# Kernel optimization log

Hardware: AMD Instinct MI355X
Metric: run time of the kernel (lower is better)

The kernel has to match this reference:

```python
import jax, jax.numpy as jnp
import numpy as np

N, D = 16384, 512
LOGIT_SCALE = 14.285714  # 1/0.07, standard CLIP temperature


def setup_inputs() -> dict:
    key = jax.random.key(0)
    k1, k2 = jax.random.split(key)
    image_features = jax.random.normal(k1, (N, D), dtype=jnp.float32)
    text_features = jax.random.normal(k2, (N, D), dtype=jnp.float32)
    logit_scale = jnp.asarray(LOGIT_SCALE, dtype=jnp.float32)
    return {
        "image_features": image_features,
        "text_features": text_features,
        "logit_scale": logit_scale,
    }


def reference(image_features, text_features, logit_scale):
    # logits_per_image = scale * img @ txt.T  -> [N, N]
    # logits_per_text is its transpose, so compute the GEMM once.
    logits = logit_scale * jnp.einsum("nd,md->nm", image_features, text_features)
    diag = jnp.diagonal(logits)  # correct-pair logits (labels = arange)
    # cross_entropy with label i on row i: logsumexp(row) - logit[i,i]
    loss_i = jnp.mean(jax.nn.logsumexp(logits, axis=1) - diag)
    # text loss uses transposed logits -> column-wise logsumexp
    loss_t = jnp.mean(jax.nn.logsumexp(logits, axis=0) - diag)
    return (loss_i + loss_t) * 0.5
```

## Files before the change

kernel.cpp:

```cpp
#include <hip/hip_runtime.h>
#include <hip/hip_bf16.h>

#define N_ 16384
#define D_ 512
#define BM 128
#define BN 128
#define BK 64
#define NBLK (N_ / BM)

typedef __attribute__((ext_vector_type(8))) __bf16 bf16x8;
typedef __attribute__((ext_vector_type(4))) float f32x4;

#define GLDS(gptr, lptr)                                                              \
  __builtin_amdgcn_global_load_lds((const __attribute__((address_space(1))) void*)(gptr), \
                                   (__attribute__((address_space(3))) void*)(lptr), 16, 0, 0)

__device__ inline unsigned short f2bf(float f) {
  __hip_bfloat16 h = __float2bfloat16(f);
  return *reinterpret_cast<unsigned short*>(&h);
}

__global__ void cvt_bf16_kernel(const float* __restrict__ src,
                                unsigned short* __restrict__ dst, long n,
                                const float* __restrict__ scale_p) {
  const float s = scale_p ? scale_p[0] : 1.0f;
  long i = ((long)blockIdx.x * blockDim.x + threadIdx.x) * 8;
  const long stride = (long)gridDim.x * blockDim.x * 8;
  typedef __attribute__((ext_vector_type(8))) unsigned short us8;
  for (; i < n; i += stride) {
    const float4* sp = (const float4*)(src + i);
    float4 f0 = sp[0], f1 = sp[1];
    us8 v;
    v[0] = f2bf(f0.x * s); v[1] = f2bf(f0.y * s); v[2] = f2bf(f0.z * s); v[3] = f2bf(f0.w * s);
    v[4] = f2bf(f1.x * s); v[5] = f2bf(f1.y * s); v[6] = f2bf(f1.z * s); v[7] = f2bf(f1.w * s);
    *(us8*)(dst + i) = v;
  }
}

__global__ __launch_bounds__(256, 4)
void gemm_lse_kernel(const unsigned short* __restrict__ A,
                     const unsigned short* __restrict__ B,
                     float2* __restrict__ rowMS,
                     float2* __restrict__ colMS,
                     float* __restrict__ diag) {
  __shared__ unsigned short As[BM][BK];
  __shared__ unsigned short Bs[BN][BK];
  __shared__ float rowbuf[2][BM][2];
  __shared__ float colbuf[2][BN][2];

  const int t = threadIdx.x;
  const int l = t & 63;
  const int wid = t >> 6;
  const int wr = wid >> 1;
  const int wc = wid & 1;

  int id = blockIdx.x;
  id = (id & 7) * (NBLK * NBLK / 8) + (id >> 3);
  const int br = id / NBLK;
  const int bc = id % NBLK;

  const int srow = t >> 3;
  const int scol = (((t & 7) ^ (srow & 7)) << 3);

  f32x4 acc[4][4];
#pragma unroll
  for (int m = 0; m < 4; ++m)
#pragma unroll
    for (int n = 0; n < 4; ++n) acc[m][n] = (f32x4)0.0f;

  const unsigned short* aBase = A + (size_t)(br * BM + srow) * D_ + scol;
  const unsigned short* bBase = B + (size_t)(bc * BN + srow) * D_ + scol;
  char* asBase = (char*)&As[0][0] + t * 16;
  char* bsBase = (char*)&Bs[0][0] + t * 16;

  const int swz = (l & 7) << 4;

  for (int kt = 0; kt < D_ / BK; ++kt) {
    const int k0 = kt * BK;
#pragma unroll
    for (int c = 0; c < 4; ++c) GLDS(aBase + k0 + c * 32 * D_, asBase + c * 4096);
#pragma unroll
    for (int c = 0; c < 4; ++c) GLDS(bBase + k0 + c * 32 * D_, bsBase + c * 4096);
    __syncthreads();
#pragma unroll
    for (int kk = 0; kk < 2; ++kk) {
      const int cb = (kk * 64 + (l >> 4) * 16);
      bf16x8 af[4], bfv[4];
#pragma unroll
      for (int m = 0; m < 4; ++m)
        af[m] = *(const bf16x8*)((const char*)&As[0][0] +
                                 (wr * 64 + m * 16 + (l & 15)) * 128 + (cb ^ swz));
#pragma unroll
      for (int n = 0; n < 4; ++n)
        bfv[n] = *(const bf16x8*)((const char*)&Bs[0][0] +
                                  (wc * 64 + n * 16 + (l & 15)) * 128 + (cb ^ swz));
#pragma unroll
      for (int m = 0; m < 4; ++m)
#pragma unroll
        for (int n = 0; n < 4; ++n)
          acc[m][n] = __builtin_amdgcn_mfma_f32_16x16x32_bf16(af[m], bfv[n], acc[m][n], 0, 0, 0);
    }
    __syncthreads();
  }

  if (br == bc && wr == wc) {
#pragma unroll
    for (int m = 0; m < 4; ++m)
#pragma unroll
      for (int r = 0; r < 4; ++r)
        if ((l & 15) == ((l >> 4) * 4 + r))
          diag[br * BM + wr * 64 + m * 16 + (l & 15)] = acc[m][m][r];
  }

#pragma unroll
  for (int m = 0; m < 4; ++m) {
#pragma unroll
    for (int r = 0; r < 4; ++r) {
      float mx = fmaxf(fmaxf(acc[m][0][r], acc[m][1][r]), fmaxf(acc[m][2][r], acc[m][3][r]));
#pragma unroll
      for (int off = 1; off < 16; off <<= 1) mx = fmaxf(mx, __shfl_xor(mx, off, 64));
      float s = 0.f;
#pragma unroll
      for (int n = 0; n < 4; ++n) s += __expf(acc[m][n][r] - mx);
#pragma unroll
      for (int off = 1; off < 16; off <<= 1) s += __shfl_xor(s, off, 64);
      if ((l & 15) == 0) {
        int row = wr * 64 + m * 16 + (l >> 4) * 4 + r;
        rowbuf[wc][row][0] = mx;
        rowbuf[wc][row][1] = s;
      }
    }
  }

#pragma unroll
  for (int n = 0; n < 4; ++n) {
    float mx = -1e30f;
#pragma unroll
    for (int m = 0; m < 4; ++m)
#pragma unroll
      for (int r = 0; r < 4; ++r) mx = fmaxf(mx, acc[m][n][r]);
    mx = fmaxf(mx, __shfl_xor(mx, 16, 64));
    mx = fmaxf(mx, __shfl_xor(mx, 32, 64));
    float s = 0.f;
#pragma unroll
    for (int m = 0; m < 4; ++m)
#pragma unroll
      for (int r = 0; r < 4; ++r) s += __expf(acc[m][n][r] - mx);
    s += __shfl_xor(s, 16, 64);
    s += __shfl_xor(s, 32, 64);
    if ((l >> 4) == 0) {
      int col = wc * 64 + n * 16 + l;
      colbuf[wr][col][0] = mx;
      colbuf[wr][col][1] = s;
    }
  }
  __syncthreads();

  if (t < BM) {
    float m0 = rowbuf[0][t][0], s0 = rowbuf[0][t][1];
    float m1 = rowbuf[1][t][0], s1 = rowbuf[1][t][1];
    float mm = fmaxf(m0, m1);
    float ss = s0 * __expf(m0 - mm) + s1 * __expf(m1 - mm);
    rowMS[(size_t)bc * N_ + br * BM + t] = make_float2(mm, ss);
  } else {
    int c = t - BM;
    float m0 = colbuf[0][c][0], s0 = colbuf[0][c][1];
    float m1 = colbuf[1][c][0], s1 = colbuf[1][c][1];
    float mm = fmaxf(m0, m1);
    float ss = s0 * __expf(m0 - mm) + s1 * __expf(m1 - mm);
    colMS[(size_t)br * N_ + bc * BN + c] = make_float2(mm, ss);
  }
}

__global__ void reduce1_kernel(const float2* __restrict__ rowMS,
                               const float2* __restrict__ colMS,
                               const float* __restrict__ diag,
                               float* __restrict__ partials) {
  const int tid = blockIdx.x * blockDim.x + threadIdx.x;
  float m = -1e30f, s = 0.f;
  if (tid < N_) {
    const int r = tid;
    for (int cb = 0; cb < NBLK; ++cb) {
      float2 p = rowMS[(size_t)cb * N_ + r];
      float nm = fmaxf(m, p.x);
      s = s * __expf(m - nm) + p.y * __expf(p.x - nm);
      m = nm;
    }
    m = m + logf(s) - diag[r];
  } else {
    const int c = tid - N_;
    for (int rb = 0; rb < NBLK; ++rb) {
      float2 p = colMS[(size_t)rb * N_ + c];
      float nm = fmaxf(m, p.x);
      s = s * __expf(m - nm) + p.y * __expf(p.x - nm);
      m = nm;
    }
    m = m + logf(s) - diag[c];
  }
  float val = m;
#pragma unroll
  for (int off = 1; off < 64; off <<= 1) val += __shfl_xor(val, off, 64);
  __shared__ float red[4];
  if ((threadIdx.x & 63) == 0) red[threadIdx.x >> 6] = val;
  __syncthreads();
  if (threadIdx.x == 0) partials[blockIdx.x] = red[0] + red[1] + red[2] + red[3];
}

__global__ void reduce2_kernel(const float* __restrict__ partials, float* __restrict__ out) {
  const int t = threadIdx.x;
  float v = partials[t] + partials[t + 64];
#pragma unroll
  for (int off = 1; off < 64; off <<= 1) v += __shfl_xor(v, off, 64);
  if (t == 0) out[0] = v * (1.0f / (2.0f * (float)N_));
}

extern "C" void kernel_launch(void* const* d_in, const int* in_sizes, int n_in,
                              void* d_out, int out_size, void* d_ws, size_t ws_size,
                              hipStream_t stream) {
  const float* img = (const float*)d_in[0];
  const float* txt = (const float*)d_in[1];
  const float* scale = (const float*)d_in[2];
  float* out = (float*)d_out;

  char* ws = (char*)d_ws;
  size_t off = 0;
  unsigned short* imgB = (unsigned short*)(ws + off); off += (size_t)N_ * D_ * 2;
  unsigned short* txtB = (unsigned short*)(ws + off); off += (size_t)N_ * D_ * 2;
  float2* rowMS = (float2*)(ws + off); off += (size_t)NBLK * N_ * sizeof(float2);
  float2* colMS = (float2*)(ws + off); off += (size_t)NBLK * N_ * sizeof(float2);
  float* diag = (float*)(ws + off); off += (size_t)N_ * sizeof(float);
  float* partials = (float*)(ws + off); off += 128 * sizeof(float);
  (void)ws_size; (void)in_sizes; (void)n_in; (void)out_size;

  cvt_bf16_kernel<<<1024, 256, 0, stream>>>(img, imgB, (long)N_ * D_, scale);
  cvt_bf16_kernel<<<1024, 256, 0, stream>>>(txt, txtB, (long)N_ * D_, nullptr);
  gemm_lse_kernel<<<NBLK * NBLK, 256, 0, stream>>>(imgB, txtB, rowMS, colMS, diag);
  reduce1_kernel<<<(2 * N_) / 256, 256, 0, stream>>>(rowMS, colMS, diag, partials);
  reduce2_kernel<<<1, 64, 0, stream>>>(partials, out);
}
```

Measured before the change: 408.7 us.

## Enlarge GEMM tile to 256x256 with 512 threads and double-buffered async LDS loads

Grows the block tile from 128x128 to 256x256 using 8 waves, each computing a 128x64 sub-tile. LDS staging is now double-buffered, with a prefetch two k-steps ahead, explicit vmcnt waits and raw barriers, so global-to-LDS copies overlap the MFMA work. MFMA sections also run at raised wave priority. This aims to cut global traffic per FLOP and hide load latency, at the cost of more registers, lower occupancy, and fewer blocks for load balance. The per-tile row/column partial LSE outputs halve in count, and the tail merge now combines four row partials instead of two.

```diff
diff --git a/kernel.cpp b/kernel.cpp
--- a/kernel.cpp
+++ b/kernel.cpp
@@ -3,10 +3,12 @@
 
 #define N_ 16384
 #define D_ 512
-#define BM 128
-#define BN 128
+#define BM 256
+#define BN 256
 #define BK 64
+#define NT (D_ / BK)
 #define NBLK (N_ / BM)
+#define BUFB 32768
 
 typedef __attribute__((ext_vector_type(8))) __bf16 bf16x8;
 typedef __attribute__((ext_vector_type(4))) float f32x4;
@@ -37,22 +39,20 @@
   }
 }
 
-__global__ __launch_bounds__(256, 4)
+__global__ __launch_bounds__(512, 2)
 void gemm_lse_kernel(const unsigned short* __restrict__ A,
                      const unsigned short* __restrict__ B,
                      float2* __restrict__ rowMS,
                      float2* __restrict__ colMS,
                      float* __restrict__ diag) {
-  __shared__ unsigned short As[BM][BK];
-  __shared__ unsigned short Bs[BN][BK];
-  __shared__ float rowbuf[2][BM][2];
-  __shared__ float colbuf[2][BN][2];
+  __shared__ __align__(16) unsigned short As[2][BM][BK];
+  __shared__ __align__(16) unsigned short Bs[2][BN][BK];
 
   const int t = threadIdx.x;
   const int l = t & 63;
   const int wid = t >> 6;
-  const int wr = wid >> 1;
-  const int wc = wid & 1;
+  const int wr = wid >> 2;
+  const int wc = wid & 3;
 
   int id = blockIdx.x;
   id = (id & 7) * (NBLK * NBLK / 8) + (id >> 3);
@@ -62,58 +62,90 @@
   const int srow = t >> 3;
   const int scol = (((t & 7) ^ (srow & 7)) << 3);
 
-  f32x4 acc[4][4];
-#pragma unroll
-  for (int m = 0; m < 4; ++m)
-#pragma unroll
-    for (int n = 0; n < 4; ++n) acc[m][n] = (f32x4)0.0f;
-
   const unsigned short* aBase = A + (size_t)(br * BM + srow) * D_ + scol;
   const unsigned short* bBase = B + (size_t)(bc * BN + srow) * D_ + scol;
-  char* asBase = (char*)&As[0][0] + t * 16;
-  char* bsBase = (char*)&Bs[0][0] + t * 16;
+
+  f32x4 acc[8][4];
+#pragma unroll
+  for (int m = 0; m < 8; ++m)
+#pragma unroll
+    for (int n = 0; n < 4; ++n) acc[m][n] = (f32x4)0.0f;
 
   const int swz = (l & 7) << 4;
-
-  for (int kt = 0; kt < D_ / BK; ++kt) {
-    const int k0 = kt * BK;
-#pragma unroll
-    for (int c = 0; c < 4; ++c) GLDS(aBase + k0 + c * 32 * D_, asBase + c * 4096);
-#pragma unroll
-    for (int c = 0; c < 4; ++c) GLDS(bBase + k0 + c * 32 * D_, bsBase + c * 4096);
-    __syncthreads();
+  const char* asb = (const char*)As;
+  const char* bsb = (const char*)Bs;
+
+#define STAGE(kt_, b_)                                              \
+  {                                                                 \
+    const unsigned short* ag_ = aBase + (kt_)*BK;                   \
+    const unsigned short* bg_ = bBase + (kt_)*BK;                   \
+    char* al_ = (char*)As + (b_)*BUFB + t * 16;                     \
+    char* bl_ = (char*)Bs + (b_)*BUFB + t * 16;                     \
+    _Pragma("unroll") for (int c_ = 0; c_ < 4; ++c_) {              \
+      GLDS(ag_ + c_ * 64 * D_, al_ + c_ * 8192);                    \
+      GLDS(bg_ + c_ * 64 * D_, bl_ + c_ * 8192);                    \
+    }                                                               \
+  }
+
+  STAGE(0, 0);
+  STAGE(1, 1);
+
+#pragma unroll
+  for (int kt = 0; kt < NT; ++kt) {
+    const int b = kt & 1;
+    if (kt == NT - 1) { asm volatile("s_waitcnt vmcnt(0)" ::: "memory"); }
+    else              { asm volatile("s_waitcnt vmcnt(8)" ::: "memory"); }
+    __builtin_amdgcn_sched_barrier(0);
+    __builtin_amdgcn_s_barrier();
+    __builtin_amdgcn_sched_barrier(0);
+
 #pragma unroll
     for (int kk = 0; kk < 2; ++kk) {
-      const int cb = (kk * 64 + (l >> 4) * 16);
-      bf16x8 af[4], bfv[4];
-#pragma unroll
-      for (int m = 0; m < 4; ++m)
-        af[m] = *(const bf16x8*)((const char*)&As[0][0] +
-                                 (wr * 64 + m * 16 + (l & 15)) * 128 + (cb ^ swz));
+      const int cbk = kk * 64 + (l >> 4) * 16;
+      bf16x8 af[8], bfv[4];
+#pragma unroll
+      for (int m = 0; m < 8; ++m)
+        af[m] = *(const bf16x8*)(asb + b * BUFB +
+                                 (wr * 128 + m * 16 + (l & 15)) * 128 + (cbk ^ swz));
 #pragma unroll
       for (int n = 0; n < 4; ++n)
-        bfv[n] = *(const bf16x8*)((const char*)&Bs[0][0] +
-                                  (wc * 64 + n * 16 + (l & 15)) * 128 + (cb ^ swz));
-#pragma unroll
-      for (int m = 0; m < 4; ++m)
+        bfv[n] = *(const bf16x8*)(bsb + b * BUFB +
+                                  (wc * 64 + n * 16 + (l & 15)) * 128 + (cbk ^ swz));
+      __builtin_amdgcn_s_setprio(1);
+#pragma unroll
+      for (int m = 0; m < 8; ++m)
 #pragma unroll
         for (int n = 0; n < 4; ++n)
           acc[m][n] = __builtin_amdgcn_mfma_f32_16x16x32_bf16(af[m], bfv[n], acc[m][n], 0, 0, 0);
-    }
-    __syncthreads();
-  }
-
-  if (br == bc && wr == wc) {
-#pragma unroll
-    for (int m = 0; m < 4; ++m)
-#pragma unroll
-      for (int r = 0; r < 4; ++r)
-        if ((l & 15) == ((l >> 4) * 4 + r))
-          diag[br * BM + wr * 64 + m * 16 + (l & 15)] = acc[m][m][r];
-  }
-
-#pragma unroll
-  for (int m = 0; m < 4; ++m) {
+      __builtin_amdgcn_s_setprio(0);
+    }
+
+    asm volatile("s_waitcnt lgkmcnt(0)" ::: "memory");
+    __builtin_amdgcn_sched_barrier(0);
+    __builtin_amdgcn_s_barrier();
+    __builtin_amdgcn_sched_barrier(0);
+    if (kt + 2 < NT) STAGE(kt + 2, b);
+  }
+#undef STAGE
+
+  float* rowb = (float*)As;
+  float* colb = rowb + 4 * 256 * 2;
+
+  if (br == bc) {
+#pragma unroll
+    for (int m = 0; m < 8; ++m)
+#pragma unroll
+      for (int n = 0; n < 4; ++n)
+#pragma unroll
+        for (int r = 0; r < 4; ++r) {
+          const int row = wr * 128 + m * 16 + (l >> 4) * 4 + r;
+          const int col = wc * 64 + n * 16 + (l & 15);
+          if (row == col) diag[br * BM + row] = acc[m][n][r];
+        }
+  }
+
+#pragma unroll
+  for (int m = 0; m < 8; ++m) {
 #pragma unroll
     for (int r = 0; r < 4; ++r) {
       float mx = fmaxf(fmaxf(acc[m][0][r], acc[m][1][r]), fmaxf(acc[m][2][r], acc[m][3][r]));
@@ -125,9 +157,9 @@
 #pragma unroll
       for (int off = 1; off < 16; off <<= 1) s += __shfl_xor(s, off, 64);
       if ((l & 15) == 0) {
-        int row = wr * 64 + m * 16 + (l >> 4) * 4 + r;
-        rowbuf[wc][row][0] = mx;
-        rowbuf[wc][row][1] = s;
+        const int row = wr * 128 + m * 16 + (l >> 4) * 4 + r;
+        rowb[(wc * 256 + row) * 2 + 0] = mx;
+        rowb[(wc * 256 + row) * 2 + 1] = s;
       }
     }
   }
@@ -136,38 +168,46 @@
   for (int n = 0; n < 4; ++n) {
     float mx = -1e30f;
 #pragma unroll
-    for (int m = 0; m < 4; ++m)
+    for (int m = 0; m < 8; ++m)
 #pragma unroll
       for (int r = 0; r < 4; ++r) mx = fmaxf(mx, acc[m][n][r]);
     mx = fmaxf(mx, __shfl_xor(mx, 16, 64));
     mx = fmaxf(mx, __shfl_xor(mx, 32, 64));
     float s = 0.f;
 #pragma unroll
-    for (int m = 0; m < 4; ++m)
+    for (int m = 0; m < 8; ++m)
 #pragma unroll
       for (int r = 0; r < 4; ++r) s += __expf(acc[m][n][r] - mx);
     s += __shfl_xor(s, 16, 64);
     s += __shfl_xor(s, 32, 64);
     if ((l >> 4) == 0) {
-      int col = wc * 64 + n * 16 + l;
-      colbuf[wr][col][0] = mx;
-      colbuf[wr][col][1] = s;
+      const int col = wc * 64 + n * 16 + l;
+      colb[(wr * 256 + col) * 2 + 0] = mx;
+      colb[(wr * 256 + col) * 2 + 1] = s;
     }
   }
   __syncthreads();
 
-  if (t < BM) {
-    float m0 = rowbuf[0][t][0], s0 = rowbuf[0][t][1];
-    float m1 = rowbuf[1][t][0], s1 = rowbuf[1][t][1];
-    float mm = fmaxf(m0, m1);
-    float ss = s0 * __expf(m0 - mm) + s1 * __expf(m1 - mm);
+  if (t < 256) {
+    float mm = -1e30f, ss = 0.f;
+#pragma unroll
+    for (int w = 0; w < 4; ++w) {
+      float m0 = rowb[(w * 256 + t) * 2 + 0], s0 = rowb[(w * 256 + t) * 2 + 1];
+      float nm = fmaxf(mm, m0);
+      ss = ss * __expf(mm - nm) + s0 * __expf(m0 - nm);
+      mm = nm;
+    }
     rowMS[(size_t)bc * N_ + br * BM + t] = make_float2(mm, ss);
   } else {
-    int c = t - BM;
-    float m0 = colbuf[0][c][0], s0 = colbuf[0][c][1];
-    float m1 = colbuf[1][c][0], s1 = colbuf[1][c][1];
-    float mm = fmaxf(m0, m1);
-    float ss = s0 * __expf(m0 - mm) + s1 * __expf(m1 - mm);
+    const int c = t - 256;
+    float mm = -1e30f, ss = 0.f;
+#pragma unroll
+    for (int w = 0; w < 2; ++w) {
+      float m0 = colb[(w * 256 + c) * 2 + 0], s0 = colb[(w * 256 + c) * 2 + 1];
+      float nm = fmaxf(mm, m0);
+      ss = ss * __expf(mm - nm) + s0 * __expf(m0 - nm);
+      mm = nm;
+    }
     colMS[(size_t)br * N_ + bc * BN + c] = make_float2(mm, ss);
   }
 }
@@ -234,7 +274,7 @@
 
   cvt_bf16_kernel<<<1024, 256, 0, stream>>>(img, imgB, (long)N_ * D_, scale);
   cvt_bf16_kernel<<<1024, 256, 0, stream>>>(txt, txtB, (long)N_ * D_, nullptr);
-  gemm_lse_kernel<<<NBLK * NBLK, 256, 0, stream>>>(imgB, txtB, rowMS, colMS, diag);
+  gemm_lse_kernel<<<NBLK * NBLK, 512, 0, stream>>>(imgB, txtB, rowMS, colMS, diag);
   reduce1_kernel<<<(2 * N_) / 256, 256, 0, stream>>>(rowMS, colMS, diag, partials);
   reduce2_kernel<<<1, 64, 0, stream>>>(partials, out);
 }
```

Measured after the change: 468.7 us. 1.15x slower.

## Double-buffer GEMM LDS tiles with BK=32 and switch LSE to base-2 exponent

Applied to the files above, without the earlier changes.

Halves the K tile to 32 and double-buffers the A/B shared tiles, so the next tile's global-to-LDS load is issued before the MFMAs on the current one. This cuts one barrier per K step and sets wave priority around the MFMA block. It also drops the XOR swizzle, which may bring LDS bank conflicts back on the fragment reads. Separately, log2(e) is folded into the bf16 conversion scale so every exp/log becomes exp2f/log2f, and the result is converted back with ln2 at the end.

```diff
diff --git a/kernel.cpp b/kernel.cpp
--- a/kernel.cpp
+++ b/kernel.cpp
@@ -5,8 +5,10 @@
 #define D_ 512
 #define BM 128
 #define BN 128
-#define BK 64
+#define BK 32
+#define NT (D_ / BK)
 #define NBLK (N_ / BM)
+#define BUFB 8192
 
 typedef __attribute__((ext_vector_type(8))) __bf16 bf16x8;
 typedef __attribute__((ext_vector_type(4))) float f32x4;
@@ -15,6 +17,8 @@
   __builtin_amdgcn_global_load_lds((const __attribute__((address_space(1))) void*)(gptr), \
                                    (__attribute__((address_space(3))) void*)(lptr), 16, 0, 0)
 
+#define MFMA16(a, b, c) __builtin_amdgcn_mfma_f32_16x16x32_bf16((a), (b), (c), 0, 0, 0)
+
 __device__ inline unsigned short f2bf(float f) {
   __hip_bfloat16 h = __float2bfloat16(f);
   return *reinterpret_cast<unsigned short*>(&h);
@@ -23,7 +27,7 @@
 __global__ void cvt_bf16_kernel(const float* __restrict__ src,
                                 unsigned short* __restrict__ dst, long n,
                                 const float* __restrict__ scale_p) {
-  const float s = scale_p ? scale_p[0] : 1.0f;
+  const float s = scale_p ? scale_p[0] * 1.4426950408889634f : 1.0f;
   long i = ((long)blockIdx.x * blockDim.x + threadIdx.x) * 8;
   const long stride = (long)gridDim.x * blockDim.x * 8;
   typedef __attribute__((ext_vector_type(8))) unsigned short us8;
@@ -43,8 +47,8 @@
                      float2* __restrict__ rowMS,
                      float2* __restrict__ colMS,
                      float* __restrict__ diag) {
-  __shared__ unsigned short As[BM][BK];
-  __shared__ unsigned short Bs[BN][BK];
+  __shared__ __align__(16) unsigned short As[2][BM][BK];
+  __shared__ __align__(16) unsigned short Bs[2][BN][BK];
   __shared__ float rowbuf[2][BM][2];
   __shared__ float colbuf[2][BN][2];
 
@@ -59,49 +63,54 @@
   const int br = id / NBLK;
   const int bc = id % NBLK;
 
-  const int srow = t >> 3;
-  const int scol = (((t & 7) ^ (srow & 7)) << 3);
-
-  f32x4 acc[4][4];
-#pragma unroll
-  for (int m = 0; m < 4; ++m)
-#pragma unroll
-    for (int n = 0; n < 4; ++n) acc[m][n] = (f32x4)0.0f;
+  const int srow = t >> 2;
+  const int scol = (t & 3) * 8;
 
   const unsigned short* aBase = A + (size_t)(br * BM + srow) * D_ + scol;
   const unsigned short* bBase = B + (size_t)(bc * BN + srow) * D_ + scol;
-  char* asBase = (char*)&As[0][0] + t * 16;
-  char* bsBase = (char*)&Bs[0][0] + t * 16;
-
-  const int swz = (l & 7) << 4;
-
-  for (int kt = 0; kt < D_ / BK; ++kt) {
-    const int k0 = kt * BK;
-#pragma unroll
-    for (int c = 0; c < 4; ++c) GLDS(aBase + k0 + c * 32 * D_, asBase + c * 4096);
-#pragma unroll
-    for (int c = 0; c < 4; ++c) GLDS(bBase + k0 + c * 32 * D_, bsBase + c * 4096);
+
+  f32x4 acc[4][4];
+#pragma unroll
+  for (int m = 0; m < 4; ++m)
+#pragma unroll
+    for (int n = 0; n < 4; ++n) acc[m][n] = (f32x4)0.0f;
+
+#define STAGE(kt_, b_)                                   \
+  {                                                      \
+    const unsigned short* ag_ = aBase + (kt_)*BK;        \
+    const unsigned short* bg_ = bBase + (kt_)*BK;        \
+    char* al_ = (char*)As + (b_)*BUFB + t * 16;          \
+    char* bl_ = (char*)Bs + (b_)*BUFB + t * 16;          \
+    GLDS(ag_, al_);                                      \
+    GLDS(ag_ + 64 * D_, al_ + 4096);                     \
+    GLDS(bg_, bl_);                                      \
+    GLDS(bg_ + 64 * D_, bl_ + 4096);                     \
+  }
+
+  STAGE(0, 0);
+  __syncthreads();
+
+#pragma unroll
+  for (int kt = 0; kt < NT; ++kt) {
+    const int cur = kt & 1;
+    if (kt + 1 < NT) STAGE(kt + 1, cur ^ 1);
+    bf16x8 af[4], bfv[4];
+#pragma unroll
+    for (int m = 0; m < 4; ++m)
+      af[m] = *(const bf16x8*)&As[cur][wr * 64 + m * 16 + (l & 15)][(l >> 4) * 8];
+#pragma unroll
+    for (int n = 0; n < 4; ++n)
+      bfv[n] = *(const bf16x8*)&Bs[cur][wc * 64 + n * 16 + (l & 15)][(l >> 4) * 8];
+    __builtin_amdgcn_s_setprio(1);
+#pragma unroll
+    for (int m = 0; m < 4; ++m)
+#pragma unroll
+      for (int n = 0; n < 4; ++n)
+        acc[m][n] = MFMA16(af[m], bfv[n], acc[m][n]);
+    __builtin_amdgcn_s_setprio(0);
     __syncthreads();
-#pragma unroll
-    for (int kk = 0; kk < 2; ++kk) {
-      const int cb = (kk * 64 + (l >> 4) * 16);
-      bf16x8 af[4], bfv[4];
-#pragma unroll
-      for (int m = 0; m < 4; ++m)
-        af[m] = *(const bf16x8*)((const char*)&As[0][0] +
-                                 (wr * 64 + m * 16 + (l & 15)) * 128 + (cb ^ swz));
-#pragma unroll
-      for (int n = 0; n < 4; ++n)
-        bfv[n] = *(const bf16x8*)((const char*)&Bs[0][0] +
-                                  (wc * 64 + n * 16 + (l & 15)) * 128 + (cb ^ swz));
-#pragma unroll
-      for (int m = 0; m < 4; ++m)
-#pragma unroll
-        for (int n = 0; n < 4; ++n)
-          acc[m][n] = __builtin_amdgcn_mfma_f32_16x16x32_bf16(af[m], bfv[n], acc[m][n], 0, 0, 0);
-    }
-    __syncthreads();
-  }
+  }
+#undef STAGE
 
   if (br == bc && wr == wc) {
 #pragma unroll
@@ -121,11 +130,11 @@
       for (int off = 1; off < 16; off <<= 1) mx = fmaxf(mx, __shfl_xor(mx, off, 64));
       float s = 0.f;
 #pragma unroll
-      for (int n = 0; n < 4; ++n) s += __expf(acc[m][n][r] - mx);
+      for (int n = 0; n < 4; ++n) s += exp2f(acc[m][n][r] - mx);
 #pragma unroll
       for (int off = 1; off < 16; off <<= 1) s += __shfl_xor(s, off, 64);
       if ((l & 15) == 0) {
-        int row = wr * 64 + m * 16 + (l >> 4) * 4 + r;
+        const int row = wr * 64 + m * 16 + (l >> 4) * 4 + r;
         rowbuf[wc][row][0] = mx;
         rowbuf[wc][row][1] = s;
       }
@@ -145,11 +154,11 @@
 #pragma unroll
     for (int m = 0; m < 4; ++m)
 #pragma unroll
-      for (int r = 0; r < 4; ++r) s += __expf(acc[m][n][r] - mx);
+      for (int r = 0; r < 4; ++r) s += exp2f(acc[m][n][r] - mx);
     s += __shfl_xor(s, 16, 64);
     s += __shfl_xor(s, 32, 64);
     if ((l >> 4) == 0) {
-      int col = wc * 64 + n * 16 + l;
+      const int col = wc * 64 + n * 16 + l;
       colbuf[wr][col][0] = mx;
       colbuf[wr][col][1] = s;
     }
@@ -160,14 +169,14 @@
     float m0 = rowbuf[0][t][0], s0 = rowbuf[0][t][1];
     float m1 = rowbuf[1][t][0], s1 = rowbuf[1][t][1];
     float mm = fmaxf(m0, m1);
-    float ss = s0 * __expf(m0 - mm) + s1 * __expf(m1 - mm);
+    float ss = s0 * exp2f(m0 - mm) + s1 * exp2f(m1 - mm);
     rowMS[(size_t)bc * N_ + br * BM + t] = make_float2(mm, ss);
   } else {
-    int c = t - BM;
+    const int c = t - BM;
     float m0 = colbuf[0][c][0], s0 = colbuf[0][c][1];
     float m1 = colbuf[1][c][0], s1 = colbuf[1][c][1];
     float mm = fmaxf(m0, m1);
-    float ss = s0 * __expf(m0 - mm) + s1 * __expf(m1 - mm);
+    float ss = s0 * exp2f(m0 - mm) + s1 * exp2f(m1 - mm);
     colMS[(size_t)br * N_ + bc * BN + c] = make_float2(mm, ss);
   }
 }
@@ -183,19 +192,19 @@
     for (int cb = 0; cb < NBLK; ++cb) {
       float2 p = rowMS[(size_t)cb * N_ + r];
       float nm = fmaxf(m, p.x);
-      s = s * __expf(m - nm) + p.y * __expf(p.x - nm);
+      s = s * exp2f(m - nm) + p.y * exp2f(p.x - nm);
       m = nm;
     }
-    m = m + logf(s) - diag[r];
+    m = m + log2f(s) - diag[r];
   } else {
     const int c = tid - N_;
     for (int rb = 0; rb < NBLK; ++rb) {
       float2 p = colMS[(size_t)rb * N_ + c];
       float nm = fmaxf(m, p.x);
-      s = s * __expf(m - nm) + p.y * __expf(p.x - nm);
+      s = s * exp2f(m - nm) + p.y * exp2f(p.x - nm);
       m = nm;
     }
-    m = m + logf(s) - diag[c];
+    m = m + log2f(s) - diag[c];
   }
   float val = m;
 #pragma unroll
@@ -211,7 +220,7 @@
   float v = partials[t] + partials[t + 64];
 #pragma unroll
   for (int off = 1; off < 64; off <<= 1) v += __shfl_xor(v, off, 64);
-  if (t == 0) out[0] = v * (1.0f / (2.0f * (float)N_));
+  if (t == 0) out[0] = v * (0.69314718055994531f / (2.0f * (float)N_));
 }
 
 extern "C" void kernel_launch(void* const* d_in, const int* in_sizes, int n_in,
```

After: 482.0 us. 1.18x slower.
